# Performance work log

Hardware: AMD Instinct MI355X
Metric: run time of the kernel (lower is better)

## Reference

```python
import jax, jax.numpy as jnp
import numpy as np

B, T, N, D, F, ORDER = 16, 12, 1024, 64, 64, 2
EPS = 1e-5  # BatchNorm eps (eval mode, running stats)


def setup_inputs() -> dict:
    key = jax.random.key(0)
    ks = jax.random.split(key, 8)
    C_eff = (ORDER + 1) * D  # (order*support_len + 1) * c_in = 192
    return {
        "x": jax.random.normal(ks[0], (B, T, N, D), jnp.float32),
        "A": jax.random.uniform(ks[1], (B, N, N), jnp.float32),  # dynamic per-sample adjacency
        "conv_w": jax.random.normal(ks[2], (F, C_eff), jnp.float32) / np.float32(np.sqrt(C_eff)),
        "conv_b": jnp.zeros((F,), jnp.float32),
        "bn_gamma": jnp.ones((F,), jnp.float32),
        "bn_beta": jnp.zeros((F,), jnp.float32),
        "bn_mean": 0.1 * jax.random.normal(ks[3], (F,), jnp.float32),
        "bn_var": jax.random.uniform(ks[4], (F,), jnp.float32) + 0.5,
        "gru_ff_w": jax.random.normal(ks[5], (T, 2 * F, 2 * F), jnp.float32) / np.float32(np.sqrt(2 * F)),
        "gru_ff_b": jnp.zeros((T, 2 * F), jnp.float32),
        "gru_zff_w": jax.random.normal(ks[6], (T, 2 * F, F), jnp.float32) / np.float32(np.sqrt(2 * F)),
        "gru_zff_b": jnp.zeros((T, F), jnp.float32),
    }


def _forward(x, A, conv_w, conv_b, bn_gamma, bn_beta, bn_mean, bn_var,
             gru_ff_w, gru_ff_b, gru_zff_w, gru_zff_b):
    # ---- DiffusionGraphEncoder ----
    xt = jnp.transpose(x, (0, 3, 2, 1))  # (B, C, N, T), matches torch transpose(1,3)
    outs = [xt]
    cur = xt
    for _ in range(ORDER):  # nconv: einsum('ncvl,nwv->ncwl')
        cur = jnp.einsum('bcvt,bwv->bcwt', cur, A)
        outs.append(cur)
    h = jnp.concatenate(outs, axis=1)        # (B, 3C, N, T)
    h = jnp.transpose(h, (0, 3, 2, 1))       # (B, T, N, C_eff)
    # ---- MLP1x1: 1x1 conv + eval-mode BatchNorm + relu ----
    y = jnp.einsum('btnc,fc->btnf', h, conv_w) + conv_b
    y = (y - bn_mean) * jax.lax.rsqrt(bn_var + EPS) * bn_gamma + bn_beta
    y = jax.nn.relu(y)  # dropout is identity at inference
    # ---- GRUEncoder: distinct GRUCellLite per timestep ----
    xs = jnp.transpose(y, (1, 0, 2, 3))      # (T, B, N, F)
    h0 = jnp.zeros((B, N, F), y.dtype)

    def step(hprev, inp):
        xt_, wff, bff, wzff, bzff = inp
        ru = jax.nn.sigmoid(jnp.concatenate([xt_, hprev], -1) @ wff + bff)
        r, u = ru[..., :F], ru[..., F:]
        z = jnp.tanh(jnp.concatenate([xt_, r * hprev], -1) @ wzff + bzff)
        hn = u * z + (1.0 - u) * hprev
        return hn, hn

    _, hs = jax.lax.scan(step, h0, (xs, gru_ff_w, gru_ff_b, gru_zff_w, gru_zff_b))
    return jnp.transpose(hs, (1, 0, 2, 3))   # (B, T, N, F)


def reference(x, A, conv_w, conv_b, bn_gamma, bn_beta, bn_mean, bn_var,
              gru_ff_w, gru_ff_b, gru_zff_w, gru_zff_b):
    return _forward(x, A, conv_w, conv_b, bn_gamma, bn_beta, bn_mean, bn_var,
                    gru_ff_w, gru_ff_b, gru_zff_w, gru_zff_b)
```

## Files before the change

### kernel.cpp

```cpp
#include <hip/hip_runtime.h>
#include <cstdint>
#include <cstddef>

#define NB 16
#define TT 12
#define NN 1024
#define DD 64
#define FF 64
#define JT 768

typedef __attribute__((ext_vector_type(8))) short v8s;
typedef __attribute__((ext_vector_type(4))) short v4s;
typedef __attribute__((ext_vector_type(4))) float v4f;

__device__ __forceinline__ float sigmoidf_(float v) { return 1.0f / (1.0f + expf(-v)); }

__device__ __forceinline__ float bf2f(unsigned short h) {
    union { unsigned int u; float f; } x; x.u = ((unsigned int)h) << 16; return x.f;
}
__device__ __forceinline__ unsigned short f2bf(float f) {
    union { float f; unsigned int u; } x; x.f = f;
    return (unsigned short)((x.u + 0x7fffu + ((x.u >> 16) & 1u)) >> 16);
}

__device__ __forceinline__ void gload16(const void* g, void* lds) {
    __builtin_amdgcn_global_load_lds(
        (const __attribute__((address_space(1))) void*)g,
        (__attribute__((address_space(3))) void*)lds, 16, 0, 0);
}

__global__ __launch_bounds__(256) void split_A(
    const float* __restrict__ A, unsigned short* __restrict__ Ah,
    unsigned short* __restrict__ Al)
{
    const size_t i0 = ((size_t)blockIdx.x * 256 + threadIdx.x) * 16;
    float v[16];
#pragma unroll
    for (int s = 0; s < 4; ++s)
        *(float4*)&v[s * 4] = *(const float4*)&A[i0 + s * 4];
    v8s h0, h1, l0, l1;
#pragma unroll
    for (int q = 0; q < 8; ++q) {
        unsigned short h = f2bf(v[q]);
        h0[q] = (short)h; l0[q] = (short)f2bf(v[q] - bf2f(h));
    }
#pragma unroll
    for (int q = 0; q < 8; ++q) {
        unsigned short h = f2bf(v[8 + q]);
        h1[q] = (short)h; l1[q] = (short)f2bf(v[8 + q] - bf2f(h));
    }
    *(v8s*)&Ah[i0] = h0; *(v8s*)&Ah[i0 + 8] = h1;
    *(v8s*)&Al[i0] = l0; *(v8s*)&Al[i0 + 8] = l1;
}

__global__ __launch_bounds__(256) void xsplitT(
    const float* __restrict__ x, unsigned short* __restrict__ Th,
    unsigned short* __restrict__ Tl)
{
    __shared__ float tile[64][68];
    const int v0 = blockIdx.x * 64, t = blockIdx.y, b = blockIdx.z;
    const int tid = threadIdx.x;
    {
        const int r = tid >> 2, q = (tid & 3) * 16;
#pragma unroll
        for (int s = 0; s < 4; ++s) {
            const float4 w = *(const float4*)&x[(((size_t)b * TT + t) * NN + v0 + r) * DD + q + s * 4];
            tile[r][q + s * 4 + 0] = w.x; tile[r][q + s * 4 + 1] = w.y;
            tile[r][q + s * 4 + 2] = w.z; tile[r][q + s * 4 + 3] = w.w;
        }
    }
    __syncthreads();
    {
        const int d = tid >> 2, vc = (tid & 3) * 16;
        const size_t base = ((size_t)b * JT + t * 64 + d) * 1024 + v0 + vc;
        v8s h0, h1, l0, l1;
#pragma unroll
        for (int s = 0; s < 8; ++s) {
            const float f = tile[vc + s][d];
            unsigned short h = f2bf(f);
            h0[s] = (short)h; l0[s] = (short)f2bf(f - bf2f(h));
        }
#pragma unroll
        for (int s = 0; s < 8; ++s) {
            const float f = tile[vc + 8 + s][d];
            unsigned short h = f2bf(f);
            h1[s] = (short)h; l1[s] = (short)f2bf(f - bf2f(h));
        }
        *(v8s*)&Th[base] = h0; *(v8s*)&Th[base + 8] = h1;
        *(v8s*)&Tl[base] = l0; *(v8s*)&Tl[base + 8] = l1;
    }
}

template<bool PAIROUT>
__global__ __launch_bounds__(256, 2) void gemm_bf(
    const unsigned short* __restrict__ Ah, const unsigned short* __restrict__ Al,
    const unsigned short* __restrict__ Bh, const unsigned short* __restrict__ Bl,
    unsigned short* __restrict__ Ch, unsigned short* __restrict__ Cl,
    float* __restrict__ Cf)
{
    __shared__ unsigned short LA[2][2][4096];
    __shared__ unsigned short LB[2][2][4096];

    const int wg = blockIdx.x;
    const int nlin = (wg & 7) * 96 + (wg >> 3);
    const int b  = nlin / 48;
    const int rr = nlin % 48;
    const int m0 = (rr / 6) * 128, n0 = (rr % 6) * 128;

    const int tid = threadIdx.x, lane = tid & 63, wid = tid >> 6;
    const int lr = lane & 15, hi = lane >> 4;
    const int wr = wid >> 1, wc = wid & 1;

    auto stage = [&](int buf, int kt) {
        const int rA = lane >> 2, kc = (lane & 3) * 8;
#pragma unroll
        for (int p = 0; p < 2; ++p) {
            const int c = wid * 2 + p;
            const size_t ga = ((size_t)b * 1024 + m0 + c * 16 + rA) * 1024 + kt * 32 + kc;
            gload16(Ah + ga, &LA[buf][0][c * 512]);
            gload16(Al + ga, &LA[buf][1][c * 512]);
            const size_t gb = ((size_t)b * JT + n0 + c * 16 + rA) * 1024 + kt * 32 + kc;
            gload16(Bh + gb, &LB[buf][0][c * 512]);
            gload16(Bl + gb, &LB[buf][1][c * 512]);
        }
    };

    v4f acc[4][4];
#pragma unroll
    for (int i = 0; i < 4; ++i)
#pragma unroll
        for (int j = 0; j < 4; ++j) acc[i][j] = (v4f){0.f, 0.f, 0.f, 0.f};

    stage(0, 0);
    __syncthreads();
    int cur = 0;
    for (int kt = 0; kt < 32; ++kt) {
        if (kt + 1 < 32) stage(cur ^ 1, kt + 1);
        v8s ah[4], al[4], bh[4], bl[4];
#pragma unroll
        for (int f = 0; f < 4; ++f) {
            const int m = wr * 64 + f * 16 + lr;
            ah[f] = *(const v8s*)&LA[cur][0][m * 32 + hi * 8];
            al[f] = *(const v8s*)&LA[cur][1][m * 32 + hi * 8];
        }
#pragma unroll
        for (int f = 0; f < 4; ++f) {
            const int n = wc * 64 + f * 16 + lr;
            bh[f] = *(const v8s*)&LB[cur][0][n * 32 + hi * 8];
            bl[f] = *(const v8s*)&LB[cur][1][n * 32 + hi * 8];
        }
#pragma unroll
        for (int fi = 0; fi < 4; ++fi)
#pragma unroll
            for (int fj = 0; fj < 4; ++fj) {
                acc[fi][fj] = __builtin_amdgcn_mfma_f32_16x16x32_bf16(ah[fi], bh[fj], acc[fi][fj], 0, 0, 0);
                acc[fi][fj] = __builtin_amdgcn_mfma_f32_16x16x32_bf16(ah[fi], bl[fj], acc[fi][fj], 0, 0, 0);
                acc[fi][fj] = __builtin_amdgcn_mfma_f32_16x16x32_bf16(al[fi], bh[fj], acc[fi][fj], 0, 0, 0);
                acc[fi][fj] = __builtin_amdgcn_mfma_f32_16x16x32_bf16(al[fi], bl[fj], acc[fi][fj], 0, 0, 0);
            }
        __syncthreads();
        cur ^= 1;
    }

#pragma unroll
    for (int fi = 0; fi < 4; ++fi)
#pragma unroll
        for (int fj = 0; fj < 4; ++fj) {
            const int n  = n0 + wc * 64 + fj * 16 + lr;
            const int mb = m0 + wr * 64 + fi * 16 + hi * 4;
            const size_t o = ((size_t)b * JT + n) * 1024 + mb;
            if (PAIROUT) {
                v4s vh, vl;
#pragma unroll
                for (int r = 0; r < 4; ++r) {
                    const float v = acc[fi][fj][r];
                    const unsigned short h = f2bf(v);
                    vh[r] = (short)h; vl[r] = (short)f2bf(v - bf2f(h));
                }
                *(v4s*)&Ch[o] = vh;
                *(v4s*)&Cl[o] = vl;
            } else {
                float4 v = {acc[fi][fj][0], acc[fi][fj][1], acc[fi][fj][2], acc[fi][fj][3]};
                *(float4*)&Cf[o] = v;
            }
        }
}

template<bool XFROMX>
__global__ __launch_bounds__(256, 4) void gemm_f32(
    const float* __restrict__ Aop, const float* __restrict__ Xin,
    float* __restrict__ Xout)
{
    __shared__ float As[2][16 * 132];
    __shared__ float Bs[2][16 * 128];
    const int wg  = blockIdx.x;
    const int nlin = (wg & 7) * 96 + (wg >> 3);
    const int b  = nlin / 48;
    const int rr = nlin % 48;
    const int rb = rr / 6, cb = rr % 6;
    const int w0 = rb * 128, j0 = cb * 128;
    const int tid = threadIdx.x;
    const int rg = tid >> 4, cg = tid & 15;
    const int row0 = rg * 8;

    auto stage = [&](int buf, int kt) {
        const float* Ab = Aop + (size_t)b * NN * NN;
#pragma unroll
        for (int p = 0; p < 2; ++p) {
            const int c  = tid + p * 256;
            const int w  = c >> 2;
            const int k4 = (c & 3) * 4;
            const float4 v = *(const float4*)&Ab[(size_t)(w0 + w) * NN + kt * 16 + k4];
            As[buf][(k4 + 0) * 132 + w] = v.x;
            As[buf][(k4 + 1) * 132 + w] = v.y;
            As[buf][(k4 + 2) * 132 + w] = v.z;
            As[buf][(k4 + 3) * 132 + w] = v.w;
        }
#pragma unroll
        for (int p = 0; p < 2; ++p) {
            const int c = tid + p * 256;
            const int k = c >> 5;
            const int j = (c & 31) * 4;
            float4 v;
            if (XFROMX) {
                const int t = cb * 2 + (j >> 6);
                const int d = j & 63;
                v = *(const float4*)&Xin[(((size_t)b * TT + t) * NN + (size_t)kt * 16 + k) * DD + d];
            } else {
                v = *(const float4*)&Xin[((size_t)b * NN + (size_t)kt * 16 + k) * JT + j0 + j];
            }
            *(float4*)&Bs[buf][k * 128 + j] = v;
        }
    };

    float acc[8][8];
#pragma unroll
    for (int i = 0; i < 8; ++i)
#pragma unroll
        for (int j = 0; j < 8; ++j) acc[i][j] = 0.0f;

    stage(0, 0);
    __syncthreads();
    int cur = 0;
    for (int kt = 0; kt < 64; ++kt) {
        if (kt + 1 < 64) stage(cur ^ 1, kt + 1);
#pragma unroll
        for (int k = 0; k < 16; ++k) {
            float a[8], bb[8];
            *(float4*)&a[0]  = *(const float4*)&As[cur][k * 132 + row0];
            *(float4*)&a[4]  = *(const float4*)&As[cur][k * 132 + row0 + 4];
            *(float4*)&bb[0] = *(const float4*)&Bs[cur][k * 128 + cg * 4];
            *(float4*)&bb[4] = *(const float4*)&Bs[cur][k * 128 + 64 + cg * 4];
#pragma unroll
            for (int i = 0; i < 8; ++i)
#pragma unroll
                for (int j = 0; j < 8; ++j)
                    acc[i][j] = fmaf(a[i], bb[j], acc[i][j]);
        }
        __syncthreads();
        cur ^= 1;
    }
#pragma unroll
    for (int i = 0; i < 8; ++i) {
        float4 v0 = {acc[i][0], acc[i][1], acc[i][2], acc[i][3]};
        float4 v1 = {acc[i][4], acc[i][5], acc[i][6], acc[i][7]};
        float* dst = Xout + ((size_t)b * NN + w0 + row0 + i) * JT + j0;
        *(float4*)&dst[cg * 4]      = v0;
        *(float4*)&dst[64 + cg * 4] = v1;
    }
}

template<bool PAIRS>
__global__ __launch_bounds__(256) void conv_bn_relu(
    const float* __restrict__ x,
    const unsigned short* __restrict__ X1h, const unsigned short* __restrict__ X1l,
    const float* __restrict__ X2T,
    const float* __restrict__ X1f, const float* __restrict__ X2f,
    const float* __restrict__ W,
    const float* __restrict__ convb, const float* __restrict__ gamma,
    const float* __restrict__ beta,  const float* __restrict__ mean,
    const float* __restrict__ var,   float* __restrict__ y)
{
    __shared__ float As[64][132];
    __shared__ float Ws[64][68];
    const int nb = blockIdx.x, t = blockIdx.y, b = blockIdx.z;
    const int n0 = nb * 128;
    const int tid = threadIdx.x;
    const int rg = tid >> 4, cg = tid & 15;
    const int row0 = rg * 8, f0 = cg * 4;

    float acc[8][4];
#pragma unroll
    for (int i = 0; i < 8; ++i)
#pragma unroll
        for (int j = 0; j < 4; ++j) acc[i][j] = 0.0f;

    for (int kt = 0; kt < 3; ++kt) {
        __syncthreads();
        if (kt == 0) {
            const float* src = x + (((size_t)b * TT + t) * NN + n0) * DD;
#pragma unroll
            for (int p = 0; p < 8; ++p) {
                const int row = (tid >> 4) + p * 16;
                const int c4  = (tid & 15) * 4;
                const float4 v = *(const float4*)&src[(size_t)row * DD + c4];
                As[c4 + 0][row] = v.x; As[c4 + 1][row] = v.y;
                As[c4 + 2][row] = v.z; As[c4 + 3][row] = v.w;
            }
        } else if (PAIRS) {
            if (kt == 1) {
#pragma unroll
                for (int p = 0; p < 4; ++p) {
                    const int pos = p * 256 + tid;
                    const int c = pos >> 4, rw = (pos & 15) * 8;
                    const size_t o = ((size_t)b * JT + t * 64 + c) * 1024 + n0 + rw;
                    const v8s hv = *(const v8s*)&X1h[o];
                    const v8s lv = *(const v8s*)&X1l[o];
#pragma unroll
                    for (int q = 0; q < 8; ++q)
                        As[c][rw + q] = bf2f((unsigned short)hv[q]) + bf2f((unsigned short)lv[q]);
                }
            } else {
#pragma unroll
                for (int p = 0; p < 8; ++p) {
                    const int pos = p * 256 + tid;
                    const int c = pos >> 5, rw = (pos & 31) * 4;
                    const float4 v = *(const float4*)&X2T[((size_t)b * JT + t * 64 + c) * 1024 + n0 + rw];
                    As[c][rw + 0] = v.x; As[c][rw + 1] = v.y;
                    As[c][rw + 2] = v.z; As[c][rw + 3] = v.w;
                }
            }
        } else {
            const float* src = ((kt == 1) ? X1f : X2f) + ((size_t)b * NN + n0) * JT + t * DD;
#pragma unroll
            for (int p = 0; p < 8; ++p) {
                const int row = (tid >> 4) + p * 16;
                const int c4  = (tid & 15) * 4;
                const float4 v = *(const float4*)&src[(size_t)row * JT + c4];
                As[c4 + 0][row] = v.x; As[c4 + 1][row] = v.y;
                As[c4 + 2][row] = v.z; As[c4 + 3][row] = v.w;
            }
        }
#pragma unroll
        for (int p = 0; p < 4; ++p) {
            const int f  = (tid >> 4) + p * 16;
            const int c4 = (tid & 15) * 4;
            const float4 v = *(const float4*)&W[f * 192 + kt * 64 + c4];
            Ws[c4 + 0][f] = v.x; Ws[c4 + 1][f] = v.y;
            Ws[c4 + 2][f] = v.z; Ws[c4 + 3][f] = v.w;
        }
        __syncthreads();
#pragma unroll
        for (int k = 0; k < 64; ++k) {
            float a[8], w[4];
            *(float4*)&a[0] = *(const float4*)&As[k][row0];
            *(float4*)&a[4] = *(const float4*)&As[k][row0 + 4];
            *(float4*)&w[0] = *(const float4*)&Ws[k][f0];
#pragma unroll
            for (int i = 0; i < 8; ++i)
#pragma unroll
                for (int j = 0; j < 4; ++j)
                    acc[i][j] = fmaf(a[i], w[j], acc[i][j]);
        }
    }
    float s[4], off[4];
#pragma unroll
    for (int j = 0; j < 4; ++j) {
        const int f = f0 + j;
        const float sc = gamma[f] / sqrtf(var[f] + 1e-5f);
        s[j]   = sc;
        off[j] = (convb[f] - mean[f]) * sc + beta[f];
    }
#pragma unroll
    for (int i = 0; i < 8; ++i) {
        float4 v;
        v.x = fmaxf(acc[i][0] * s[0] + off[0], 0.0f);
        v.y = fmaxf(acc[i][1] * s[1] + off[1], 0.0f);
        v.z = fmaxf(acc[i][2] * s[2] + off[2], 0.0f);
        v.w = fmaxf(acc[i][3] * s[3] + off[3], 0.0f);
        *(float4*)&y[(((size_t)b * TT + t) * NN + n0 + row0 + i) * FF + f0] = v;
    }
}

__global__ __launch_bounds__(256) void wprep3(
    const float* __restrict__ wff, const float* __restrict__ wzff,
    unsigned short* __restrict__ WF, unsigned short* __restrict__ WZ)
{
    const int t = blockIdx.x;
    unsigned short* F = WF + (size_t)t * 40960;
    for (int e = threadIdx.x; e < 8192; e += 256) {
        const int o = e >> 6, k = e & 63;
        const float vx = wff[((size_t)t * 128 + k) * 128 + o];
        const unsigned short xh = f2bf(vx);
        const float r1 = vx - bf2f(xh);
        const unsigned short xm = f2bf(r1);
        const unsigned short xl = f2bf(r1 - bf2f(xm));
        F[0 * 8192 + o * 64 + k] = xh;
        F[1 * 8192 + o * 64 + k] = xm;
        F[2 * 8192 + o * 64 + k] = xl;
        const float vh = wff[((size_t)t * 128 + 64 + k) * 128 + o];
        const unsigned short hh = f2bf(vh);
        const unsigned short hl = f2bf(vh - bf2f(hh));
        F[3 * 8192 + o * 64 + k] = hh;
        F[4 * 8192 + o * 64 + k] = hl;
    }
    unsigned short* Z = WZ + (size_t)t * 20480;
    for (int e = threadIdx.x; e < 4096; e += 256) {
        const int o = e >> 6, k = e & 63;
        const float vx = wzff[((size_t)t * 128 + k) * 64 + o];
        const unsigned short xh = f2bf(vx);
        const float r1 = vx - bf2f(xh);
        const unsigned short xm = f2bf(r1);
        const unsigned short xl = f2bf(r1 - bf2f(xm));
        Z[0 * 4096 + o * 64 + k] = xh;
        Z[1 * 4096 + o * 64 + k] = xm;
        Z[2 * 4096 + o * 64 + k] = xl;
        const float vr = wzff[((size_t)t * 128 + 64 + k) * 64 + o];
        const unsigned short rh = f2bf(vr);
        const unsigned short rl = f2bf(vr - bf2f(rh));
        Z[3 * 4096 + o * 64 + k] = rh;
        Z[4 * 4096 + o * 64 + k] = rl;
    }
}

__global__ __launch_bounds__(256, 2) void gru4(
    const float* __restrict__ y,
    const unsigned short* __restrict__ WF, const unsigned short* __restrict__ WZ,
    const float* __restrict__ bff, const float* __restrict__ bzff,
    float* __restrict__ out)
{
    __shared__ unsigned short Ahp[4096];
    __shared__ unsigned short Rhp[4096];
    __shared__ float Hs[32][68];

    const int tid = threadIdx.x, lane = tid & 63, w = tid >> 6;
    const int lr = lane & 15, hi = lane >> 4;
    const int b = blockIdx.x >> 5, n0 = (blockIdx.x & 31) * 32;

    for (int i = tid; i < 4096; i += 256) { Ahp[i] = 0; Rhp[i] = 0; }
    for (int i = tid; i < 32 * 68; i += 256) (&Hs[0][0])[i] = 0.0f;
    __syncthreads();

    for (int t = 0; t < TT; ++t) {
        v8s xa[2][2][3];
        const float* yb = y + (((size_t)b * TT + t) * NN + n0) * 64;
#pragma unroll
        for (int mf = 0; mf < 2; ++mf)
#pragma unroll
            for (int kc = 0; kc < 2; ++kc) {
                const int m = mf * 16 + lr;
                float xv[8];
                *(float4*)&xv[0] = *(const float4*)&yb[m * 64 + kc * 32 + hi * 8];
                *(float4*)&xv[4] = *(const float4*)&yb[m * 64 + kc * 32 + hi * 8 + 4];
                v8s h3, m3, l3;
#pragma unroll
                for (int q = 0; q < 8; ++q) {
                    const float v = xv[q];
                    const unsigned short hh = f2bf(v);
                    const float r1 = v - bf2f(hh);
                    const unsigned short mm = f2bf(r1);
                    const unsigned short ll = f2bf(r1 - bf2f(mm));
                    h3[q] = (short)hh; m3[q] = (short)mm; l3[q] = (short)ll;
                }
                xa[mf][kc][0] = h3; xa[mf][kc][1] = m3; xa[mf][kc][2] = l3;
            }
        v8s ha[2][2][2];
#pragma unroll
        for (int mf = 0; mf < 2; ++mf)
#pragma unroll
            for (int kc = 0; kc < 2; ++kc) {
                const int m = mf * 16 + lr;
                const int base = m * 128 + kc * 32 + hi * 8;
                const int sw = (m & 7) << 3;
                ha[mf][kc][0] = *(const v8s*)&Ahp[base ^ sw];
                ha[mf][kc][1] = *(const v8s*)&Ahp[(base + 64) ^ sw];
            }
        __syncthreads();

        v4f acc[2][2];
#pragma unroll
        for (int of = 0; of < 2; ++of)
#pragma unroll
            for (int mf = 0; mf < 2; ++mf) acc[of][mf] = (v4f){0.f, 0.f, 0.f, 0.f};

#pragma unroll
        for (int of = 0; of < 2; ++of) {
            const int o = (2 * w + of) * 16 + lr;
            v8s wx[2][3], wh_[2][2];
#pragma unroll
            for (int kc = 0; kc < 2; ++kc) {
#pragma unroll
                for (int lev = 0; lev < 3; ++lev)
                    wx[kc][lev] = *(const v8s*)&WF[((size_t)t * 5 + lev) * 8192 + o * 64 + kc * 32 + hi * 8];
#pragma unroll
                for (int lev = 0; lev < 2; ++lev)
                    wh_[kc][lev] = *(const v8s*)&WF[((size_t)t * 5 + 3 + lev) * 8192 + o * 64 + kc * 32 + hi * 8];
            }
#pragma unroll
            for (int mf = 0; mf < 2; ++mf)
#pragma unroll
                for (int kc = 0; kc < 2; ++kc) {
                    v4f a = acc[of][mf];
                    a = __builtin_amdgcn_mfma_f32_16x16x32_bf16(xa[mf][kc][0], wx[kc][0], a, 0, 0, 0);
                    a = __builtin_amdgcn_mfma_f32_16x16x32_bf16(xa[mf][kc][0], wx[kc][1], a, 0, 0, 0);
                    a = __builtin_amdgcn_mfma_f32_16x16x32_bf16(xa[mf][kc][1], wx[kc][0], a, 0, 0, 0);
                    a = __builtin_amdgcn_mfma_f32_16x16x32_bf16(xa[mf][kc][0], wx[kc][2], a, 0, 0, 0);
                    a = __builtin_amdgcn_mfma_f32_16x16x32_bf16(xa[mf][kc][1], wx[kc][1], a, 0, 0, 0);
                    a = __builtin_amdgcn_mfma_f32_16x16x32_bf16(xa[mf][kc][2], wx[kc][0], a, 0, 0, 0);
                    a = __builtin_amdgcn_mfma_f32_16x16x32_bf16(ha[mf][kc][0], wh_[kc][0], a, 0, 0, 0);
                    a = __builtin_amdgcn_mfma_f32_16x16x32_bf16(ha[mf][kc][0], wh_[kc][1], a, 0, 0, 0);
                    a = __builtin_amdgcn_mfma_f32_16x16x32_bf16(ha[mf][kc][1], wh_[kc][0], a, 0, 0, 0);
                    acc[of][mf] = a;
                }
        }
        __syncthreads();

        float u_[2][2][4];
#pragma unroll
        for (int of = 0; of < 2; ++of) {
            const int o = (2 * w + of) * 16 + lr;
            const float bv = bff[(size_t)t * 128 + o];
#pragma unroll
            for (int mf = 0; mf < 2; ++mf)
#pragma unroll
                for (int q = 0; q < 4; ++q) {
                    const float g = sigmoidf_(acc[of][mf][q] + bv);
                    if (w < 2) {
                        const int m = mf * 16 + hi * 4 + q;
                        const float rh = g * Hs[m][o];
                        const unsigned short h = f2bf(rh);
                        const unsigned short l = f2bf(rh - bf2f(h));
                        const int sw = (m & 7) << 3;
                        Rhp[(m * 128 + o) ^ sw]      = h;
                        Rhp[(m * 128 + 64 + o) ^ sw] = l;
                    } else {
                        u_[of][mf][q] = g;
                    }
                }
        }
        __syncthreads();

        v8s ra[2][2][2];
#pragma unroll
        for (int mf = 0; mf < 2; ++mf)
#pragma unroll
            for (int kc = 0; kc < 2; ++kc) {
                const int m = mf * 16 + lr;
                const int base = m * 128 + kc * 32 + hi * 8;
                const int sw = (m & 7) << 3;
                ra[mf][kc][0] = *(const v8s*)&Rhp[base ^ sw];
                ra[mf][kc][1] = *(const v8s*)&Rhp[(base + 64) ^ sw];
            }
        __syncthreads();

        v4f accz[2][2];
#pragma unroll
        for (int of = 0; of < 2; ++of)
#pragma unroll
            for (int mf = 0; mf < 2; ++mf) accz[of][mf] = (v4f){0.f, 0.f, 0.f, 0.f};

#pragma unroll
        for (int of = 0; of < 2; ++of) {
            const int o = (w & 1) * 32 + of * 16 + lr;
            v8s wx[2][3], wr_[2][2];
#pragma unroll
            for (int kc = 0; kc < 2; ++kc) {
#pragma unroll
                for (int lev = 0; lev < 3; ++lev)
                    wx[kc][lev] = *(const v8s*)&WZ[((size_t)t * 5 + lev) * 4096 + o * 64 + kc * 32 + hi * 8];
#pragma unroll
                for (int lev = 0; lev < 2; ++lev)
                    wr_[kc][lev] = *(const v8s*)&WZ[((size_t)t * 5 + 3 + lev) * 4096 + o * 64 + kc * 32 + hi * 8];
            }
#pragma unroll
            for (int mf = 0; mf < 2; ++mf)
#pragma unroll
                for (int kc = 0; kc < 2; ++kc) {
                    v4f a = accz[of][mf];
                    a = __builtin_amdgcn_mfma_f32_16x16x32_bf16(xa[mf][kc][0], wx[kc][0], a, 0, 0, 0);
                    a = __builtin_amdgcn_mfma_f32_16x16x32_bf16(xa[mf][kc][0], wx[kc][1], a, 0, 0, 0);
                    a = __builtin_amdgcn_mfma_f32_16x16x32_bf16(xa[mf][kc][1], wx[kc][0], a, 0, 0, 0);
                    a = __builtin_amdgcn_mfma_f32_16x16x32_bf16(xa[mf][kc][0], wx[kc][2], a, 0, 0, 0);
                    a = __builtin_amdgcn_mfma_f32_16x16x32_bf16(xa[mf][kc][1], wx[kc][1], a, 0, 0, 0);
                    a = __builtin_amdgcn_mfma_f32_16x16x32_bf16(xa[mf][kc][2], wx[kc][0], a, 0, 0, 0);
                    a = __builtin_amdgcn_mfma_f32_16x16x32_bf16(ra[mf][kc][0], wr_[kc][0], a, 0, 0, 0);
                    a = __builtin_amdgcn_mfma_f32_16x16x32_bf16(ra[mf][kc][0], wr_[kc][1], a, 0, 0, 0);
                    a = __builtin_amdgcn_mfma_f32_16x16x32_bf16(ra[mf][kc][1], wr_[kc][0], a, 0, 0, 0);
                    accz[of][mf] = a;
                }
        }
        __syncthreads();

        if (w >= 2) {
#pragma unroll
            for (int of = 0; of < 2; ++of) {
                const int o = (w & 1) * 32 + of * 16 + lr;
                const float bz = bzff[(size_t)t * 64 + o];
#pragma unroll
                for (int mf = 0; mf < 2; ++mf)
#pragma unroll
                    for (int q = 0; q < 4; ++q) {
                        const int m = mf * 16 + hi * 4 + q;
                        const float z = tanhf(accz[of][mf][q] + bz);
                        const float u = u_[of][mf][q];
                        const float hn = u * z + (1.0f - u) * Hs[m][o];
                        Hs[m][o] = hn;
                        const unsigned short h = f2bf(hn);
                        const unsigned short l = f2bf(hn - bf2f(h));
                        const int sw = (m & 7) << 3;
                        Ahp[(m * 128 + o) ^ sw]      = h;
                        Ahp[(m * 128 + 64 + o) ^ sw] = l;
                        out[(((size_t)b * TT + t) * NN + n0 + m) * 64 + o] = hn;
                    }
            }
        }
        __syncthreads();
    }
}

__global__ __launch_bounds__(256) void gru_all(
    const float* __restrict__ y,    const float* __restrict__ wff,
    const float* __restrict__ bff,  const float* __restrict__ wzff,
    const float* __restrict__ bzff, float* __restrict__ out)
{
    __shared__ float Xs[64][36];
    __shared__ float Hs[64][36];
    __shared__ float Rs[64][36];
    __shared__ float Us[64][36];
    __shared__ float Ws[64][132];
    const int tid = threadIdx.x;
    const int mb  = blockIdx.x;
    const int b = mb >> 5, n0 = (mb & 31) * 32;
    const int rg = tid >> 5;
    const int og = tid & 31;

    for (int i = tid; i < 64 * 36; i += 256) (&Hs[0][0])[i] = 0.0f;

    for (int t = 0; t < TT; ++t) {
        {
            const float* xt = y + (((size_t)b * TT + t) * NN + n0) * DD;
            const int m = tid >> 3, c0 = (tid & 7) * 8;
            const float4 v0 = *(const float4*)&xt[m * DD + c0];
            const float4 v1 = *(const float4*)&xt[m * DD + c0 + 4];
            Xs[c0 + 0][m] = v0.x; Xs[c0 + 1][m] = v0.y;
            Xs[c0 + 2][m] = v0.z; Xs[c0 + 3][m] = v0.w;
            Xs[c0 + 4][m] = v1.x; Xs[c0 + 5][m] = v1.y;
            Xs[c0 + 6][m] = v1.z; Xs[c0 + 7][m] = v1.w;
        }
        float acc[4][4];
#pragma unroll
        for (int i = 0; i < 4; ++i)
#pragma unroll
            for (int j = 0; j < 4; ++j) acc[i][j] = 0.0f;

#pragma unroll
        for (int half = 0; half < 2; ++half) {
            __syncthreads();
#pragma unroll
            for (int p = 0; p < 8; ++p) {
                const int kk = (tid >> 5) + p * 8;
                const int o4 = (tid & 31) * 4;
                *(float4*)&Ws[kk][o4] =
                    *(const float4*)&wff[((size_t)t * 128 + half * 64 + kk) * 128 + o4];
            }
            __syncthreads();
            const float (*Asrc)[36] = half ? Hs : Xs;
#pragma unroll 4
            for (int kk = 0; kk < 64; ++kk) {
                const float4 av = *(const float4*)&Asrc[kk][rg * 4];
                const float4 wv = *(const float4*)&Ws[kk][og * 4];
                const float a0 = av.x, a1 = av.y, a2 = av.z, a3 = av.w;
                acc[0][0] = fmaf(a0, wv.x, acc[0][0]); acc[0][1] = fmaf(a0, wv.y, acc[0][1]);
                acc[0][2] = fmaf(a0, wv.z, acc[0][2]); acc[0][3] = fmaf(a0, wv.w, acc[0][3]);
                acc[1][0] = fmaf(a1, wv.x, acc[1][0]); acc[1][1] = fmaf(a1, wv.y, acc[1][1]);
                acc[1][2] = fmaf(a1, wv.z, acc[1][2]); acc[1][3] = fmaf(a1, wv.w, acc[1][3]);
                acc[2][0] = fmaf(a2, wv.x, acc[2][0]); acc[2][1] = fmaf(a2, wv.y, acc[2][1]);
                acc[2][2] = fmaf(a2, wv.z, acc[2][2]); acc[2][3] = fmaf(a2, wv.w, acc[2][3]);
                acc[3][0] = fmaf(a3, wv.x, acc[3][0]); acc[3][1] = fmaf(a3, wv.y, acc[3][1]);
                acc[3][2] = fmaf(a3, wv.z, acc[3][2]); acc[3][3] = fmaf(a3, wv.w, acc[3][3]);
            }
        }
        {
            const float4 bb4 = *(const float4*)&bff[(size_t)t * 128 + og * 4];
            float g[4][4];
#pragma unroll
            for (int i = 0; i < 4; ++i) {
                g[i][0] = sigmoidf_(acc[i][0] + bb4.x);
                g[i][1] = sigmoidf_(acc[i][1] + bb4.y);
                g[i][2] = sigmoidf_(acc[i][2] + bb4.z);
                g[i][3] = sigmoidf_(acc[i][3] + bb4.w);
            }
            if (og < 16) {
#pragma unroll
                for (int i = 0; i < 4; ++i)
#pragma unroll
                    for (int j = 0; j < 4; ++j) {
                        const int f = og * 4 + j, m = rg * 4 + i;
                        Rs[f][m] = g[i][j] * Hs[f][m];
                    }
            } else {
#pragma unroll
                for (int i = 0; i < 4; ++i)
#pragma unroll
                    for (int j = 0; j < 4; ++j)
                        Us[og * 4 + j - 64][rg * 4 + i] = g[i][j];
            }
        }
        float accz[4][2];
#pragma unroll
        for (int i = 0; i < 4; ++i) { accz[i][0] = 0.0f; accz[i][1] = 0.0f; }

#pragma unroll
        for (int half = 0; half < 2; ++half) {
            __syncthreads();
#pragma unroll
            for (int p = 0; p < 4; ++p) {
                const int kk = (tid >> 4) + p * 16;
                const int f4 = (tid & 15) * 4;
                *(float4*)&Ws[kk][f4] =
                    *(const float4*)&wzff[((size_t)t * 128 + half * 64 + kk) * 64 + f4];
            }
            __syncthreads();
            const float (*Asrc)[36] = half ? Rs : Xs;
#pragma unroll 4
            for (int kk = 0; kk < 64; ++kk) {
                const float4 av = *(const float4*)&Asrc[kk][rg * 4];
                const float2 wv = *(const float2*)&Ws[kk][og * 2];
                accz[0][0] = fmaf(av.x, wv.x, accz[0][0]); accz[0][1] = fmaf(av.x, wv.y, accz[0][1]);
                accz[1][0] = fmaf(av.y, wv.x, accz[1][0]); accz[1][1] = fmaf(av.y, wv.y, accz[1][1]);
                accz[2][0] = fmaf(av.z, wv.x, accz[2][0]); accz[2][1] = fmaf(av.z, wv.y, accz[2][1]);
                accz[3][0] = fmaf(av.w, wv.x, accz[3][0]); accz[3][1] = fmaf(av.w, wv.y, accz[3][1]);
            }
        }
        {
            const float2 bz = *(const float2*)&bzff[(size_t)t * 64 + og * 2];
            const int f0_ = og * 2;
#pragma unroll
            for (int i = 0; i < 4; ++i) {
                const int m = rg * 4 + i;
                const float z0 = tanhf(accz[i][0] + bz.x);
                const float z1 = tanhf(accz[i][1] + bz.y);
                const float u0 = Us[f0_][m],     u1 = Us[f0_ + 1][m];
                const float h0 = Hs[f0_][m],     h1 = Hs[f0_ + 1][m];
                const float hn0 = u0 * z0 + (1.0f - u0) * h0;
                const float hn1 = u1 * z1 + (1.0f - u1) * h1;
                Hs[f0_][m] = hn0; Hs[f0_ + 1][m] = hn1;
                *(float2*)&out[(((size_t)b * TT + t) * NN + n0 + m) * FF + f0_] =
                    make_float2(hn0, hn1);
            }
        }
        __syncthreads();
    }
}

extern "C" void kernel_launch(void* const* d_in, const int* in_sizes, int n_in,
                              void* d_out, int out_size, void* d_ws, size_t ws_size,
                              hipStream_t stream)
{
    const float* x        = (const float*)d_in[0];
    const float* A        = (const float*)d_in[1];
    const float* conv_w   = (const float*)d_in[2];
    const float* conv_b   = (const float*)d_in[3];
    const float* bn_gamma = (const float*)d_in[4];
    const float* bn_beta  = (const float*)d_in[5];
    const float* bn_mean  = (const float*)d_in[6];
    const float* bn_var   = (const float*)d_in[7];
    const float* gru_ff_w  = (const float*)d_in[8];
    const float* gru_ff_b  = (const float*)d_in[9];
    const float* gru_zff_w = (const float*)d_in[10];
    const float* gru_zff_b = (const float*)d_in[11];
    float* out = (float*)d_out;
    char* w = (char*)d_ws;

    const size_t szA_bf  = (size_t)NB * NN * NN * 2;
    const size_t szXT_bf = (size_t)NB * JT * NN * 2;
    const size_t needFast = 2 * szA_bf + 2 * szXT_bf + 2 * szXT_bf;

    dim3 gconv(8, TT, NB);

    if (ws_size >= needFast) {
        unsigned short* Ah2 = (unsigned short*)(w);
        unsigned short* Al2 = (unsigned short*)(w + szA_bf);
        unsigned short* X1h = (unsigned short*)(w + 2 * szA_bf);
        unsigned short* X1l = (unsigned short*)(w + 2 * szA_bf + szXT_bf);
        char* slot = w + 2 * szA_bf + 2 * szXT_bf;
        unsigned short* xh = (unsigned short*)slot;
        unsigned short* xl = (unsigned short*)(slot + szXT_bf);
        float* X2T = (float*)slot;
        float* yb = (float*)w;
        unsigned short* WF = (unsigned short*)(w + 50331648);
        unsigned short* WZ = (unsigned short*)(w + 50331648 + 983040);

        xsplitT<<<dim3(16, TT, NB), 256, 0, stream>>>(x, xh, xl);
        split_A<<<4096, 256, 0, stream>>>(A, Ah2, Al2);
        gemm_bf<true ><<<768, 256, 0, stream>>>(Ah2, Al2, xh,  xl,  X1h, X1l, nullptr);
        gemm_bf<false><<<768, 256, 0, stream>>>(Ah2, Al2, X1h, X1l, nullptr, nullptr, X2T);
        conv_bn_relu<true><<<gconv, 256, 0, stream>>>(x, X1h, X1l, X2T, nullptr, nullptr,
                                                      conv_w, conv_b, bn_gamma, bn_beta,
                                                      bn_mean, bn_var, yb);
        wprep3<<<TT, 256, 0, stream>>>(gru_ff_w, gru_zff_w, WF, WZ);
        gru4<<<512, 256, 0, stream>>>(yb, WF, WZ, gru_ff_b, gru_zff_b, out);
    } else {
        const size_t szX = (size_t)NB * NN * JT;
        float* X1 = (float*)w;
        float* X2 = X1 + szX;
        float* yb = X2 + szX;
        gemm_f32<true ><<<768, 256, 0, stream>>>(A, x,  X1);
        gemm_f32<false><<<768, 256, 0, stream>>>(A, X1, X2);
        conv_bn_relu<false><<<gconv, 256, 0, stream>>>(x, nullptr, nullptr, nullptr, X1, X2,
                                                       conv_w, conv_b, bn_gamma, bn_beta,
                                                       bn_mean, bn_var, yb);
        gru_all<<<512, 256, 0, stream>>>(yb, gru_ff_w, gru_ff_b,
                                         gru_zff_w, gru_zff_b, out);
    }
}
```

Baseline: 543.5 us.

## Software-pipeline GRU input projections one timestep ahead of recurrence

The GRU kernel now computes the input-dependent MFMA contributions (x·W for the r/u and z gates) for timestep t+1 while timestep t's recurrent h-dependent MFMAs run. Only the hidden-state part stays on the serial critical path between barriers. This adds register pressure from the extra accumulators and the prefetched split x operands, which could lower occupancy under the 2-blocks launch bound.

```diff
diff --git a/kernel.cpp b/kernel.cpp
--- a/kernel.cpp
+++ b/kernel.cpp
@@ -423,7 +423,7 @@
     }
 }
 
-__global__ __launch_bounds__(256, 2) void gru4(
+__global__ __launch_bounds__(256, 2) void gru5(
     const float* __restrict__ y,
     const unsigned short* __restrict__ WF, const unsigned short* __restrict__ WZ,
     const float* __restrict__ bff, const float* __restrict__ bzff,
@@ -441,8 +441,7 @@
     for (int i = tid; i < 32 * 68; i += 256) (&Hs[0][0])[i] = 0.0f;
     __syncthreads();
 
-    for (int t = 0; t < TT; ++t) {
-        v8s xa[2][2][3];
+    auto loadx = [&](int t, v8s xa[2][2][3]) {
         const float* yb = y + (((size_t)b * TT + t) * NN + n0) * 64;
 #pragma unroll
         for (int mf = 0; mf < 2; ++mf)
@@ -464,6 +463,75 @@
                 }
                 xa[mf][kc][0] = h3; xa[mf][kc][1] = m3; xa[mf][kc][2] = l3;
             }
+    };
+    auto xru_mfma = [&](int t, const v8s xa[2][2][3], v4f xacc[2][2]) {
+#pragma unroll
+        for (int of = 0; of < 2; ++of) {
+            const int o = (2 * w + of) * 16 + lr;
+            v8s wx[2][3];
+#pragma unroll
+            for (int kc = 0; kc < 2; ++kc)
+#pragma unroll
+                for (int lev = 0; lev < 3; ++lev)
+                    wx[kc][lev] = *(const v8s*)&WF[((size_t)t * 5 + lev) * 8192 + o * 64 + kc * 32 + hi * 8];
+#pragma unroll
+            for (int mf = 0; mf < 2; ++mf)
+#pragma unroll
+                for (int kc = 0; kc < 2; ++kc) {
+                    v4f a = xacc[of][mf];
+                    a = __builtin_amdgcn_mfma_f32_16x16x32_bf16(xa[mf][kc][0], wx[kc][0], a, 0, 0, 0);
+                    a = __builtin_amdgcn_mfma_f32_16x16x32_bf16(xa[mf][kc][0], wx[kc][1], a, 0, 0, 0);
+                    a = __builtin_amdgcn_mfma_f32_16x16x32_bf16(xa[mf][kc][1], wx[kc][0], a, 0, 0, 0);
+                    a = __builtin_amdgcn_mfma_f32_16x16x32_bf16(xa[mf][kc][0], wx[kc][2], a, 0, 0, 0);
+                    a = __builtin_amdgcn_mfma_f32_16x16x32_bf16(xa[mf][kc][1], wx[kc][1], a, 0, 0, 0);
+                    a = __builtin_amdgcn_mfma_f32_16x16x32_bf16(xa[mf][kc][2], wx[kc][0], a, 0, 0, 0);
+                    xacc[of][mf] = a;
+                }
+        }
+    };
+    auto xz_mfma = [&](int t, const v8s xa[2][2][3], v4f xacc[2][2]) {
+#pragma unroll
+        for (int of = 0; of < 2; ++of) {
+            const int o = (w & 1) * 32 + of * 16 + lr;
+            v8s wx[2][3];
+#pragma unroll
+            for (int kc = 0; kc < 2; ++kc)
+#pragma unroll
+                for (int lev = 0; lev < 3; ++lev)
+                    wx[kc][lev] = *(const v8s*)&WZ[((size_t)t * 5 + lev) * 4096 + o * 64 + kc * 32 + hi * 8];
+#pragma unroll
+            for (int mf = 0; mf < 2; ++mf)
+#pragma unroll
+                for (int kc = 0; kc < 2; ++kc) {
+                    v4f a = xacc[of][mf];
+                    a = __builtin_amdgcn_mfma_f32_16x16x32_bf16(xa[mf][kc][0], wx[kc][0], a, 0, 0, 0);
+                    a = __builtin_amdgcn_mfma_f32_16x16x32_bf16(xa[mf][kc][0], wx[kc][1], a, 0, 0, 0);
+                    a = __builtin_amdgcn_mfma_f32_16x16x32_bf16(xa[mf][kc][1], wx[kc][0], a, 0, 0, 0);
+                    a = __builtin_amdgcn_mfma_f32_16x16x32_bf16(xa[mf][kc][0], wx[kc][2], a, 0, 0, 0);
+                    a = __builtin_amdgcn_mfma_f32_16x16x32_bf16(xa[mf][kc][1], wx[kc][1], a, 0, 0, 0);
+                    a = __builtin_amdgcn_mfma_f32_16x16x32_bf16(xa[mf][kc][2], wx[kc][0], a, 0, 0, 0);
+                    xacc[of][mf] = a;
+                }
+        }
+    };
+
+    v4f xru[2][2], xz[2][2];
+#pragma unroll
+    for (int of = 0; of < 2; ++of)
+#pragma unroll
+        for (int mf = 0; mf < 2; ++mf) {
+            xru[of][mf] = (v4f){0.f, 0.f, 0.f, 0.f};
+            xz[of][mf]  = (v4f){0.f, 0.f, 0.f, 0.f};
+        }
+    {
+        v8s xa0[2][2][3];
+        loadx(0, xa0);
+        xru_mfma(0, xa0, xru);
+        xz_mfma(0, xa0, xz);
+    }
+
+    for (int t = 0; t < TT; ++t) {
+        const int hasNext = (t + 1 < TT);
         v8s ha[2][2][2];
 #pragma unroll
         for (int mf = 0; mf < 2; ++mf)
@@ -481,37 +549,41 @@
 #pragma unroll
         for (int of = 0; of < 2; ++of)
 #pragma unroll
-            for (int mf = 0; mf < 2; ++mf) acc[of][mf] = (v4f){0.f, 0.f, 0.f, 0.f};
-
-#pragma unroll
-        for (int of = 0; of < 2; ++of) {
-            const int o = (2 * w + of) * 16 + lr;
-            v8s wx[2][3], wh_[2][2];
-#pragma unroll
-            for (int kc = 0; kc < 2; ++kc) {
-#pragma unroll
-                for (int lev = 0; lev < 3; ++lev)
-                    wx[kc][lev] = *(const v8s*)&WF[((size_t)t * 5 + lev) * 8192 + o * 64 + kc * 32 + hi * 8];
-#pragma unroll
-                for (int lev = 0; lev < 2; ++lev)
-                    wh_[kc][lev] = *(const v8s*)&WF[((size_t)t * 5 + 3 + lev) * 8192 + o * 64 + kc * 32 + hi * 8];
-            }
-#pragma unroll
-            for (int mf = 0; mf < 2; ++mf)
-#pragma unroll
-                for (int kc = 0; kc < 2; ++kc) {
-                    v4f a = acc[of][mf];
-                    a = __builtin_amdgcn_mfma_f32_16x16x32_bf16(xa[mf][kc][0], wx[kc][0], a, 0, 0, 0);
-                    a = __builtin_amdgcn_mfma_f32_16x16x32_bf16(xa[mf][kc][0], wx[kc][1], a, 0, 0, 0);
-                    a = __builtin_amdgcn_mfma_f32_16x16x32_bf16(xa[mf][kc][1], wx[kc][0], a, 0, 0, 0);
-                    a = __builtin_amdgcn_mfma_f32_16x16x32_bf16(xa[mf][kc][0], wx[kc][2], a, 0, 0, 0);
-                    a = __builtin_amdgcn_mfma_f32_16x16x32_bf16(xa[mf][kc][1], wx[kc][1], a, 0, 0, 0);
-                    a = __builtin_amdgcn_mfma_f32_16x16x32_bf16(xa[mf][kc][2], wx[kc][0], a, 0, 0, 0);
-                    a = __builtin_amdgcn_mfma_f32_16x16x32_bf16(ha[mf][kc][0], wh_[kc][0], a, 0, 0, 0);
-                    a = __builtin_amdgcn_mfma_f32_16x16x32_bf16(ha[mf][kc][0], wh_[kc][1], a, 0, 0, 0);
-                    a = __builtin_amdgcn_mfma_f32_16x16x32_bf16(ha[mf][kc][1], wh_[kc][0], a, 0, 0, 0);
-                    acc[of][mf] = a;
-                }
+            for (int mf = 0; mf < 2; ++mf) acc[of][mf] = xru[of][mf];
+
+        v8s xan[2][2][3];
+        v4f xruN[2][2], xzN[2][2];
+#pragma unroll
+        for (int of = 0; of < 2; ++of)
+#pragma unroll
+            for (int mf = 0; mf < 2; ++mf) {
+                xruN[of][mf] = (v4f){0.f, 0.f, 0.f, 0.f};
+                xzN[of][mf]  = (v4f){0.f, 0.f, 0.f, 0.f};
+            }
+        if (hasNext) loadx(t + 1, xan);
+
+        {
+#pragma unroll
+            for (int of = 0; of < 2; ++of) {
+                const int o = (2 * w + of) * 16 + lr;
+                v8s wh_[2][2];
+#pragma unroll
+                for (int kc = 0; kc < 2; ++kc)
+#pragma unroll
+                    for (int lev = 0; lev < 2; ++lev)
+                        wh_[kc][lev] = *(const v8s*)&WF[((size_t)t * 5 + 3 + lev) * 8192 + o * 64 + kc * 32 + hi * 8];
+#pragma unroll
+                for (int mf = 0; mf < 2; ++mf)
+#pragma unroll
+                    for (int kc = 0; kc < 2; ++kc) {
+                        v4f a = acc[of][mf];
+                        a = __builtin_amdgcn_mfma_f32_16x16x32_bf16(ha[mf][kc][0], wh_[kc][0], a, 0, 0, 0);
+                        a = __builtin_amdgcn_mfma_f32_16x16x32_bf16(ha[mf][kc][0], wh_[kc][1], a, 0, 0, 0);
+                        a = __builtin_amdgcn_mfma_f32_16x16x32_bf16(ha[mf][kc][1], wh_[kc][0], a, 0, 0, 0);
+                        acc[of][mf] = a;
+                    }
+            }
+            if (hasNext) xru_mfma(t + 1, xan, xruN);
         }
         __syncthreads();
 
@@ -557,37 +629,30 @@
 #pragma unroll
         for (int of = 0; of < 2; ++of)
 #pragma unroll
-            for (int mf = 0; mf < 2; ++mf) accz[of][mf] = (v4f){0.f, 0.f, 0.f, 0.f};
-
-#pragma unroll
-        for (int of = 0; of < 2; ++of) {
-            const int o = (w & 1) * 32 + of * 16 + lr;
-            v8s wx[2][3], wr_[2][2];
-#pragma unroll
-            for (int kc = 0; kc < 2; ++kc) {
-#pragma unroll
-                for (int lev = 0; lev < 3; ++lev)
-                    wx[kc][lev] = *(const v8s*)&WZ[((size_t)t * 5 + lev) * 4096 + o * 64 + kc * 32 + hi * 8];
-#pragma unroll
-                for (int lev = 0; lev < 2; ++lev)
-                    wr_[kc][lev] = *(const v8s*)&WZ[((size_t)t * 5 + 3 + lev) * 4096 + o * 64 + kc * 32 + hi * 8];
-            }
-#pragma unroll
-            for (int mf = 0; mf < 2; ++mf)
-#pragma unroll
-                for (int kc = 0; kc < 2; ++kc) {
-                    v4f a = accz[of][mf];
-                    a = __builtin_amdgcn_mfma_f32_16x16x32_bf16(xa[mf][kc][0], wx[kc][0], a, 0, 0, 0);
-                    a = __builtin_amdgcn_mfma_f32_16x16x32_bf16(xa[mf][kc][0], wx[kc][1], a, 0, 0, 0);
-                    a = __builtin_amdgcn_mfma_f32_16x16x32_bf16(xa[mf][kc][1], wx[kc][0], a, 0, 0, 0);
-                    a = __builtin_amdgcn_mfma_f32_16x16x32_bf16(xa[mf][kc][0], wx[kc][2], a, 0, 0, 0);
-                    a = __builtin_amdgcn_mfma_f32_16x16x32_bf16(xa[mf][kc][1], wx[kc][1], a, 0, 0, 0);
-                    a = __builtin_amdgcn_mfma_f32_16x16x32_bf16(xa[mf][kc][2], wx[kc][0], a, 0, 0, 0);
-                    a = __builtin_amdgcn_mfma_f32_16x16x32_bf16(ra[mf][kc][0], wr_[kc][0], a, 0, 0, 0);
-                    a = __builtin_amdgcn_mfma_f32_16x16x32_bf16(ra[mf][kc][0], wr_[kc][1], a, 0, 0, 0);
-                    a = __builtin_amdgcn_mfma_f32_16x16x32_bf16(ra[mf][kc][1], wr_[kc][0], a, 0, 0, 0);
-                    accz[of][mf] = a;
-                }
+            for (int mf = 0; mf < 2; ++mf) accz[of][mf] = xz[of][mf];
+
+        {
+#pragma unroll
+            for (int of = 0; of < 2; ++of) {
+                const int o = (w & 1) * 32 + of * 16 + lr;
+                v8s wr_[2][2];
+#pragma unroll
+                for (int kc = 0; kc < 2; ++kc)
+#pragma unroll
+                    for (int lev = 0; lev < 2; ++lev)
+                        wr_[kc][lev] = *(const v8s*)&WZ[((size_t)t * 5 + 3 + lev) * 4096 + o * 64 + kc * 32 + hi * 8];
+#pragma unroll
+                for (int mf = 0; mf < 2; ++mf)
+#pragma unroll
+                    for (int kc = 0; kc < 2; ++kc) {
+                        v4f a = accz[of][mf];
+                        a = __builtin_amdgcn_mfma_f32_16x16x32_bf16(ra[mf][kc][0], wr_[kc][0], a, 0, 0, 0);
+                        a = __builtin_amdgcn_mfma_f32_16x16x32_bf16(ra[mf][kc][0], wr_[kc][1], a, 0, 0, 0);
+                        a = __builtin_amdgcn_mfma_f32_16x16x32_bf16(ra[mf][kc][1], wr_[kc][0], a, 0, 0, 0);
+                        accz[of][mf] = a;
+                    }
+            }
+            if (hasNext) xz_mfma(t + 1, xan, xzN);
         }
         __syncthreads();
 
@@ -615,6 +680,14 @@
             }
         }
         __syncthreads();
+
+#pragma unroll
+        for (int of = 0; of < 2; ++of)
+#pragma unroll
+            for (int mf = 0; mf < 2; ++mf) {
+                xru[of][mf] = xruN[of][mf];
+                xz[of][mf]  = xzN[of][mf];
+            }
     }
 }
 
@@ -799,7 +872,7 @@
                                                       conv_w, conv_b, bn_gamma, bn_beta,
                                                       bn_mean, bn_var, yb);
         wprep3<<<TT, 256, 0, stream>>>(gru_ff_w, gru_zff_w, WF, WZ);
-        gru4<<<512, 256, 0, stream>>>(yb, WF, WZ, gru_ff_b, gru_zff_b, out);
+        gru5<<<512, 256, 0, stream>>>(yb, WF, WZ, gru_ff_b, gru_zff_b, out);
     } else {
         const size_t szX = (size_t)NB * NN * JT;
         float* X1 = (float*)w;
```

New measurement: 512.9 us. -5.6%, faster.
